# Optimization experiments

Hardware: AMD Instinct MI355X
Metric: run time of the kernel (lower is better)

The kernel has to match this reference:

```python
import jax, jax.numpy as jnp
import numpy as np

N_NODES = 100_000
N_EDGES = 800_000
D = 96
BN_EPS = 1e-5
LEAKY_SLOPE = 0.01


def setup_inputs() -> dict:
    key = jax.random.key(0)
    ks = jax.random.split(key, 9)
    x = jax.random.normal(ks[0], (N_NODES, D), dtype=jnp.float32)
    edge_index = jax.random.randint(ks[1], (2, N_EDGES), 0, N_NODES, dtype=jnp.int64)
    s = 0.05
    return {
        "x": x,
        "edge_index": edge_index,
        # SAGEConv #1 (mean aggregator, bias=False)
        "W_self1": jax.random.normal(ks[2], (D, D), dtype=jnp.float32) * s,
        "W_neigh1": jax.random.normal(ks[3], (D, D), dtype=jnp.float32) * s,
        # SAGEConv #2 (pool aggregator): fc_pool has bias, fc_self/fc_neigh bias=False
        "W_pool": jax.random.normal(ks[4], (D, D), dtype=jnp.float32) * s,
        "b_pool": jax.random.normal(ks[5], (D,), dtype=jnp.float32) * s,
        "W_self2": jax.random.normal(ks[6], (D, D), dtype=jnp.float32) * s,
        "W_neigh2": jax.random.normal(ks[7], (D, D), dtype=jnp.float32) * s,
        # BatchNorm affine params
        "g1": jnp.ones((D,), jnp.float32),
        "beta1": jnp.zeros((D,), jnp.float32),
        "g2": jnp.ones((D,), jnp.float32),
        "beta2": jnp.zeros((D,), jnp.float32),
    }


def _batch_norm(h, gamma, beta):
    # training-mode BatchNorm1d: biased batch stats over nodes
    mu = h.mean(axis=0)
    var = jnp.mean(jnp.square(h - mu), axis=0)
    return gamma * (h - mu) * jax.lax.rsqrt(var + BN_EPS) + beta


def _forward(x, edge_index, W_self1, W_neigh1, W_pool, b_pool, W_self2, W_neigh2,
             g1, beta1, g2, beta2):
    src, dst = edge_index[0], edge_index[1]
    n = x.shape[0]
    deg = jax.ops.segment_sum(jnp.ones((src.shape[0],), x.dtype), dst, num_segments=n)

    # ---- SAGEConv (mean): h_neigh = mean_{u in N(v)} x_u ; out = x W_self + h_neigh W_neigh
    agg_sum = jax.ops.segment_sum(x[src], dst, num_segments=n)          # [N, D]
    h_mean = agg_sum / jnp.maximum(deg, 1.0)[:, None]                   # 0 for isolated nodes
    out1 = x @ W_self1 + h_mean @ W_neigh1
    out1 = _batch_norm(out1, g1, beta1)

    # ---- SAGEConv (pool): h_neigh = max_{u in N(v)} relu(x_u W_pool + b_pool)
    hp = jax.nn.relu(x @ W_pool + b_pool)                               # [N, D]
    agg_max = jax.ops.segment_max(hp[src], dst, num_segments=n)        # -inf where empty
    h_max = jnp.where(deg[:, None] > 0, agg_max, 0.0)
    out2 = x @ W_self2 + h_max @ W_neigh2
    out2 = _batch_norm(out2, g2, beta2)

    return jax.nn.leaky_relu(out1 + out2, negative_slope=LEAKY_SLOPE)


def reference(x, edge_index, W_self1, W_neigh1, W_pool, b_pool, W_self2, W_neigh2,
              g1, beta1, g2, beta2):
    return _forward(x, edge_index, W_self1, W_neigh1, W_pool, b_pool,
                    W_self2, W_neigh2, g1, beta1, g2, beta2)
```

## Files before the change

kernel.cpp:

```cpp
#include <hip/hip_runtime.h>

#define NN 100000
#define NE 800000
#define DD 96
#define NROWPAD 100096
#define GBLK 782
#define SCAN_BLOCKS 100
#define SCAN_CHUNK 1000

typedef __attribute__((ext_vector_type(8))) short bf16x8;
typedef __attribute__((ext_vector_type(8))) unsigned short u16x8;
typedef __attribute__((ext_vector_type(4))) float f32x4;
typedef unsigned short u16;
typedef unsigned int u32;

#define MFMA16 __builtin_amdgcn_mfma_f32_16x16x32_bf16

#define OFF_DEG      0u
#define OFF_ROWSTART 100000u
#define OFF_CURSOR   200004u
#define OFF_BSUM     300004u
#define OFF_STATS    300132u
#define OFF_PARAMS   300516u
#define OFF_WT       300900u
#define OFF_CSR      323940u
#define OFF_XH       1123940u
#define OFF_HMBF     10733156u
#define OFF_HXBF     15537764u

__device__ __forceinline__ u16 f2b(float f) {
  u32 u = __float_as_uint(f);
  u += 0x7FFFu + ((u >> 16) & 1u);
  return (u16)(u >> 16);
}
__device__ __forceinline__ float b2f(short h) {
  return __uint_as_float(((u32)(u16)h) << 16);
}

__global__ void wprep_kernel(const float* __restrict__ Ws1, const float* __restrict__ Wn1,
                             const float* __restrict__ Ws2, const float* __restrict__ Wn2,
                             const float* __restrict__ Wp, u16* __restrict__ wt) {
  int idx = blockIdx.x * 256 + threadIdx.x;
  if (idx >= 5 * 9216) return;
  int m = idx / 9216, r = idx % 9216;
  int k = r / 96, c = r % 96;
  const float* W = (m == 0) ? Ws1 : (m == 1) ? Wn1 : (m == 2) ? Ws2 : (m == 3) ? Wn2 : Wp;
  wt[m * 9216 + c * 96 + k] = f2b(W[k * 96 + c]);
}

__global__ void deg_kernel(const int* __restrict__ dst, int* __restrict__ deg) {
  int e = blockIdx.x * blockDim.x + threadIdx.x;
  if (e >= NE) return;
  atomicAdd(&deg[dst[e]], 1);
}

__global__ void scan_sum_kernel(const int* __restrict__ deg, int* __restrict__ bsum) {
  __shared__ int red[256];
  int t = threadIdx.x;
  int base = blockIdx.x * SCAN_CHUNK;
  int s = 0;
  for (int i = t; i < SCAN_CHUNK; i += 256) s += deg[base + i];
  red[t] = s;
  __syncthreads();
  for (int off = 128; off > 0; off >>= 1) {
    if (t < off) red[t] += red[t + off];
    __syncthreads();
  }
  if (t == 0) bsum[blockIdx.x] = red[0];
}

__global__ void scan_bsum_kernel(int* __restrict__ bsum, int* __restrict__ row_start) {
  __shared__ int sm[128];
  int t = threadIdx.x;
  int v = (t < SCAN_BLOCKS) ? bsum[t] : 0;
  sm[t] = v;
  __syncthreads();
  for (int off = 1; off < 128; off <<= 1) {
    int u = 0;
    if (t >= off) u = sm[t - off];
    __syncthreads();
    if (t >= off) sm[t] += u;
    __syncthreads();
  }
  if (t < SCAN_BLOCKS) bsum[t] = sm[t] - v;
  if (t == SCAN_BLOCKS - 1) row_start[NN] = sm[t];
}

__global__ void scan_final_kernel(const int* __restrict__ deg,
                                  const int* __restrict__ bsum,
                                  int* __restrict__ row_start,
                                  int* __restrict__ cursor) {
  __shared__ int sm[256];
  int t = threadIdx.x;
  int base = blockIdx.x * SCAN_CHUNK + t * 4;
  int4 d = {0, 0, 0, 0};
  if (t < 250) d = *reinterpret_cast<const int4*>(deg + base);
  int tot = d.x + d.y + d.z + d.w;
  sm[t] = tot;
  __syncthreads();
  for (int off = 1; off < 256; off <<= 1) {
    int u = 0;
    if (t >= off) u = sm[t - off];
    __syncthreads();
    if (t >= off) sm[t] += u;
    __syncthreads();
  }
  if (t < 250) {
    int run = bsum[blockIdx.x] + sm[t] - tot;
    int4 rs;
    rs.x = run;
    rs.y = run + d.x;
    rs.z = run + d.x + d.y;
    rs.w = run + d.x + d.y + d.z;
    *reinterpret_cast<int4*>(row_start + base) = rs;
    *reinterpret_cast<int4*>(cursor + base) = rs;
  }
}

__global__ void fill_csr_kernel(const int* __restrict__ src,
                                const int* __restrict__ dst,
                                int* __restrict__ cursor,
                                int* __restrict__ csr) {
  int e = blockIdx.x * blockDim.x + threadIdx.x;
  if (e >= NE) return;
  int pos = atomicAdd(&cursor[dst[e]], 1);
  csr[pos] = src[e];
}

__global__ __launch_bounds__(512) void hp_gemm_kernel(const float* __restrict__ x,
                                                      const u16* __restrict__ wt,
                                                      const float* __restrict__ bp,
                                                      u16* __restrict__ xh) {
  __shared__ bf16x8 wl[1152];
  int t = threadIdx.x;
  const bf16x8* wg = reinterpret_cast<const bf16x8*>(wt + 4 * 9216);
  for (int j = t; j < 1152; j += 512) wl[j] = wg[j];
  __syncthreads();
  int w = t >> 6, lane = t & 63;
  int i = lane & 15, g = lane >> 4;
  int row_base = blockIdx.x * 128 + w * 16;
  int grow_a = row_base + i;
  int lrow = grow_a < NN ? grow_a : NN - 1;
  const float4* xr = reinterpret_cast<const float4*>(x + (size_t)lrow * 96);
  bf16x8* xhv = reinterpret_cast<bf16x8*>(xh);
  bf16x8 ax[3];
#pragma unroll
  for (int kb = 0; kb < 3; ++kb) {
    float4 p = xr[(kb * 4 + g) * 2];
    float4 q = xr[(kb * 4 + g) * 2 + 1];
    bf16x8 v;
    v[0] = (short)f2b(p.x); v[1] = (short)f2b(p.y); v[2] = (short)f2b(p.z); v[3] = (short)f2b(p.w);
    v[4] = (short)f2b(q.x); v[5] = (short)f2b(q.y); v[6] = (short)f2b(q.z); v[7] = (short)f2b(q.w);
    ax[kb] = v;
    xhv[(size_t)grow_a * 24 + kb * 4 + g] = v;
  }
  for (int nt = 0; nt < 6; ++nt) {
    f32x4 acc = {0.f, 0.f, 0.f, 0.f};
    int bch = (nt * 16 + i) * 12;
#pragma unroll
    for (int kb = 0; kb < 3; ++kb)
      acc = MFMA16(ax[kb], wl[bch + kb * 4 + g], acc, 0, 0, 0);
    int col = nt * 16 + i;
    float bias = bp[col];
#pragma unroll
    for (int r = 0; r < 4; ++r) {
      int grow = row_base + g * 4 + r;
      xh[(size_t)grow * 192 + 96 + col] = f2b(fmaxf(acc[r] + bias, 0.0f));
    }
  }
}

__global__ __launch_bounds__(256) void gather_kernel(const u16* __restrict__ xh,
                                                     const int* __restrict__ row_start,
                                                     const int* __restrict__ csr,
                                                     u16* __restrict__ hmbf,
                                                     u16* __restrict__ hxbf) {
  int t = threadIdx.x;
  int node = blockIdx.x * 32 + (t & 31);
  int slot = t >> 5;
  bool isMax = slot >= 4;
  if (node >= NN) return;
  int beg = row_start[node], end = row_start[node + 1];
  int cbase = slot * 3;
  const u16x8* XH = reinterpret_cast<const u16x8*>(xh);
  float s0[8], s1[8], s2[8];
  u16x8 m0, m1, m2;
#pragma unroll
  for (int j = 0; j < 8; ++j) {
    s0[j] = 0.f; s1[j] = 0.f; s2[j] = 0.f;
    m0[j] = 0; m1[j] = 0; m2[j] = 0;
  }
  int e = beg;
  int i0 = csr[(e < end) ? e : 0];
  int i1 = csr[(e + 1 < end) ? e + 1 : ((end > beg) ? end - 1 : 0)];
  for (; e + 2 <= end; e += 2) {
    int p2 = e + 2, p3 = e + 3;
    int n0 = csr[(p2 < end) ? p2 : end - 1];
    int n1 = csr[(p3 < end) ? p3 : end - 1];
    size_t b0 = (size_t)i0 * 24 + cbase;
    size_t b1 = (size_t)i1 * 24 + cbase;
    u16x8 u0 = XH[b0], u1 = XH[b0 + 1], u2 = XH[b0 + 2];
    u16x8 v0 = XH[b1], v1 = XH[b1 + 1], v2 = XH[b1 + 2];
    if (isMax) {
#pragma unroll
      for (int j = 0; j < 8; ++j) {
        u16 a = u0[j] > v0[j] ? u0[j] : v0[j]; m0[j] = m0[j] > a ? m0[j] : a;
        u16 b = u1[j] > v1[j] ? u1[j] : v1[j]; m1[j] = m1[j] > b ? m1[j] : b;
        u16 c = u2[j] > v2[j] ? u2[j] : v2[j]; m2[j] = m2[j] > c ? m2[j] : c;
      }
    } else {
#pragma unroll
      for (int j = 0; j < 8; ++j) {
        s0[j] += b2f((short)u0[j]) + b2f((short)v0[j]);
        s1[j] += b2f((short)u1[j]) + b2f((short)v1[j]);
        s2[j] += b2f((short)u2[j]) + b2f((short)v2[j]);
      }
    }
    i0 = n0; i1 = n1;
  }
  if (e < end) {
    size_t b0 = (size_t)i0 * 24 + cbase;
    u16x8 u0 = XH[b0], u1 = XH[b0 + 1], u2 = XH[b0 + 2];
    if (isMax) {
#pragma unroll
      for (int j = 0; j < 8; ++j) {
        m0[j] = m0[j] > u0[j] ? m0[j] : u0[j];
        m1[j] = m1[j] > u1[j] ? m1[j] : u1[j];
        m2[j] = m2[j] > u2[j] ? m2[j] : u2[j];
      }
    } else {
#pragma unroll
      for (int j = 0; j < 8; ++j) {
        s0[j] += b2f((short)u0[j]);
        s1[j] += b2f((short)u1[j]);
        s2[j] += b2f((short)u2[j]);
      }
    }
  }
  if (isMax) {
    u16x8* dv = reinterpret_cast<u16x8*>(hxbf);
    size_t ob = (size_t)node * 12 + (slot - 4) * 3;
    dv[ob] = m0; dv[ob + 1] = m1; dv[ob + 2] = m2;
  } else {
    float scl = (end > beg) ? 1.0f / (float)(end - beg) : 0.0f;
    u16x8 w0, w1, w2;
#pragma unroll
    for (int j = 0; j < 8; ++j) {
      w0[j] = f2b(s0[j] * scl);
      w1[j] = f2b(s1[j] * scl);
      w2[j] = f2b(s2[j] * scl);
    }
    u16x8* dv = reinterpret_cast<u16x8*>(hmbf);
    size_t ob = (size_t)node * 12 + slot * 3;
    dv[ob] = w0; dv[ob + 1] = w1; dv[ob + 2] = w2;
  }
}

__global__ __launch_bounds__(512, 4) void stats_gemm_kernel(const u16* __restrict__ xh,
                                                            const u16* __restrict__ hmbf,
                                                            const u16* __restrict__ hxbf,
                                                            const u16* __restrict__ wt,
                                                            float* __restrict__ stats) {
  __shared__ bf16x8 wl[4608];
  __shared__ float smst[384];
  int t = threadIdx.x;
  const bf16x8* wg = reinterpret_cast<const bf16x8*>(wt);
  for (int j = t; j < 4608; j += 512) wl[j] = wg[j];
  for (int j = t; j < 384; j += 512) smst[j] = 0.f;
  __syncthreads();
  int w = t >> 6, lane = t & 63;
  int i = lane & 15, g = lane >> 4;
  int row_base = blockIdx.x * 128 + w * 16;
  size_t arowx = (size_t)(row_base + i) * 24;
  size_t arowh = (size_t)(row_base + i) * 12;
  bf16x8 ax0, ax1, ax2, am0, am1, am2, ah0, ah1, ah2;
  {
    const bf16x8* X = reinterpret_cast<const bf16x8*>(xh);
    const bf16x8* M = reinterpret_cast<const bf16x8*>(hmbf);
    const bf16x8* H = reinterpret_cast<const bf16x8*>(hxbf);
    ax0 = X[arowx + g]; ax1 = X[arowx + 4 + g]; ax2 = X[arowx + 8 + g];
    am0 = M[arowh + g]; am1 = M[arowh + 4 + g]; am2 = M[arowh + 8 + g];
    ah0 = H[arowh + g]; ah1 = H[arowh + 4 + g]; ah2 = H[arowh + 8 + g];
  }
#pragma unroll
  for (int nt = 0; nt < 6; ++nt) {
    f32x4 a1 = {0.f, 0.f, 0.f, 0.f}, a2 = {0.f, 0.f, 0.f, 0.f};
    int bch = (nt * 16 + i) * 12 + g;
    a1 = MFMA16(ax0, wl[bch], a1, 0, 0, 0);
    a1 = MFMA16(ax1, wl[bch + 4], a1, 0, 0, 0);
    a1 = MFMA16(ax2, wl[bch + 8], a1, 0, 0, 0);
    a1 = MFMA16(am0, wl[1152 + bch], a1, 0, 0, 0);
    a1 = MFMA16(am1, wl[1152 + bch + 4], a1, 0, 0, 0);
    a1 = MFMA16(am2, wl[1152 + bch + 8], a1, 0, 0, 0);
    a2 = MFMA16(ax0, wl[2304 + bch], a2, 0, 0, 0);
    a2 = MFMA16(ax1, wl[2304 + bch + 4], a2, 0, 0, 0);
    a2 = MFMA16(ax2, wl[2304 + bch + 8], a2, 0, 0, 0);
    a2 = MFMA16(ah0, wl[3456 + bch], a2, 0, 0, 0);
    a2 = MFMA16(ah1, wl[3456 + bch + 4], a2, 0, 0, 0);
    a2 = MFMA16(ah2, wl[3456 + bch + 8], a2, 0, 0, 0);
    int col = nt * 16 + i;
    float s1 = 0, q1 = 0, s2 = 0, q2 = 0;
#pragma unroll
    for (int r = 0; r < 4; ++r) {
      int grow = row_base + g * 4 + r;
      if (grow < NN) {
        float v = a1[r], u = a2[r];
        s1 += v; q1 += v * v; s2 += u; q2 += u * u;
      }
    }
    s1 += __shfl_xor(s1, 16); q1 += __shfl_xor(q1, 16);
    s2 += __shfl_xor(s2, 16); q2 += __shfl_xor(q2, 16);
    s1 += __shfl_xor(s1, 32); q1 += __shfl_xor(q1, 32);
    s2 += __shfl_xor(s2, 32); q2 += __shfl_xor(q2, 32);
    if (g == 0) {
      atomicAdd(&smst[col], s1);
      atomicAdd(&smst[96 + col], q1);
      atomicAdd(&smst[192 + col], s2);
      atomicAdd(&smst[288 + col], q2);
    }
  }
  __syncthreads();
  for (int j = t; j < 384; j += 512) atomicAdd(&stats[j], smst[j]);
}

__global__ void finalize_kernel(const float* __restrict__ stats,
                                const float* __restrict__ g1, const float* __restrict__ beta1,
                                const float* __restrict__ g2, const float* __restrict__ beta2,
                                float* __restrict__ params) {
  int c = threadIdx.x;
  if (c >= 96) return;
  const float inv_n = 1.0f / NN;
  float mu1 = stats[c] * inv_n;
  float var1 = fmaxf(stats[96 + c] * inv_n - mu1 * mu1, 0.0f);
  float is1 = rsqrtf(var1 + 1e-5f);
  float a1 = g1[c] * is1;
  params[c] = a1;
  params[96 + c] = beta1[c] - a1 * mu1;
  float mu2 = stats[192 + c] * inv_n;
  float var2 = fmaxf(stats[288 + c] * inv_n - mu2 * mu2, 0.0f);
  float is2 = rsqrtf(var2 + 1e-5f);
  float a2 = g2[c] * is2;
  params[192 + c] = a2;
  params[288 + c] = beta2[c] - a2 * mu2;
}

__global__ __launch_bounds__(512, 4) void out_gemm_kernel(const u16* __restrict__ xh,
                                                          const u16* __restrict__ hmbf,
                                                          const u16* __restrict__ hxbf,
                                                          const u16* __restrict__ wt,
                                                          const float* __restrict__ params,
                                                          float* __restrict__ out) {
  __shared__ bf16x8 wl[4608];
  __shared__ float pl[384];
  int t = threadIdx.x;
  const bf16x8* wg = reinterpret_cast<const bf16x8*>(wt);
  for (int j = t; j < 4608; j += 512) wl[j] = wg[j];
  for (int j = t; j < 384; j += 512) pl[j] = params[j];
  __syncthreads();
  int w = t >> 6, lane = t & 63;
  int i = lane & 15, g = lane >> 4;
  int row_base = blockIdx.x * 128 + w * 16;
  size_t arowx = (size_t)(row_base + i) * 24;
  size_t arowh = (size_t)(row_base + i) * 12;
  bf16x8 ax0, ax1, ax2, am0, am1, am2, ah0, ah1, ah2;
  {
    const bf16x8* X = reinterpret_cast<const bf16x8*>(xh);
    const bf16x8* M = reinterpret_cast<const bf16x8*>(hmbf);
    const bf16x8* H = reinterpret_cast<const bf16x8*>(hxbf);
    ax0 = X[arowx + g]; ax1 = X[arowx + 4 + g]; ax2 = X[arowx + 8 + g];
    am0 = M[arowh + g]; am1 = M[arowh + 4 + g]; am2 = M[arowh + 8 + g];
    ah0 = H[arowh + g]; ah1 = H[arowh + 4 + g]; ah2 = H[arowh + 8 + g];
  }
#pragma unroll
  for (int nt = 0; nt < 6; ++nt) {
    f32x4 a1 = {0.f, 0.f, 0.f, 0.f}, a2 = {0.f, 0.f, 0.f, 0.f};
    int bch = (nt * 16 + i) * 12 + g;
    a1 = MFMA16(ax0, wl[bch], a1, 0, 0, 0);
    a1 = MFMA16(ax1, wl[bch + 4], a1, 0, 0, 0);
    a1 = MFMA16(ax2, wl[bch + 8], a1, 0, 0, 0);
    a1 = MFMA16(am0, wl[1152 + bch], a1, 0, 0, 0);
    a1 = MFMA16(am1, wl[1152 + bch + 4], a1, 0, 0, 0);
    a1 = MFMA16(am2, wl[1152 + bch + 8], a1, 0, 0, 0);
    a2 = MFMA16(ax0, wl[2304 + bch], a2, 0, 0, 0);
    a2 = MFMA16(ax1, wl[2304 + bch + 4], a2, 0, 0, 0);
    a2 = MFMA16(ax2, wl[2304 + bch + 8], a2, 0, 0, 0);
    a2 = MFMA16(ah0, wl[3456 + bch], a2, 0, 0, 0);
    a2 = MFMA16(ah1, wl[3456 + bch + 4], a2, 0, 0, 0);
    a2 = MFMA16(ah2, wl[3456 + bch + 8], a2, 0, 0, 0);
    int col = nt * 16 + i;
    float p1 = pl[col], c1 = pl[96 + col];
    float p2 = pl[192 + col], c2 = pl[288 + col];
#pragma unroll
    for (int r = 0; r < 4; ++r) {
      int grow = row_base + g * 4 + r;
      if (grow < NN) {
        float v = p1 * a1[r] + c1 + p2 * a2[r] + c2;
        v = v > 0.f ? v : 0.01f * v;
        out[(size_t)grow * 96 + col] = v;
      }
    }
  }
}

extern "C" void kernel_launch(void* const* d_in, const int* in_sizes, int n_in,
                              void* d_out, int out_size, void* d_ws, size_t ws_size,
                              hipStream_t stream) {
  const float* x       = (const float*)d_in[0];
  const int*   ei      = (const int*)d_in[1];
  const float* W_self1 = (const float*)d_in[2];
  const float* W_neigh1= (const float*)d_in[3];
  const float* W_pool  = (const float*)d_in[4];
  const float* b_pool  = (const float*)d_in[5];
  const float* W_self2 = (const float*)d_in[6];
  const float* W_neigh2= (const float*)d_in[7];
  const float* g1      = (const float*)d_in[8];
  const float* beta1   = (const float*)d_in[9];
  const float* g2      = (const float*)d_in[10];
  const float* beta2   = (const float*)d_in[11];
  float* out = (float*)d_out;

  float* ws = (float*)d_ws;
  int*   deg       = (int*)(ws + OFF_DEG);
  int*   row_start = (int*)(ws + OFF_ROWSTART);
  int*   cursor    = (int*)(ws + OFF_CURSOR);
  int*   bsum      = (int*)(ws + OFF_BSUM);
  float* stats     = ws + OFF_STATS;
  float* params    = ws + OFF_PARAMS;
  u16*   wt        = (u16*)(ws + OFF_WT);
  int*   csr       = (int*)(ws + OFF_CSR);
  u16*   xh        = (u16*)(ws + OFF_XH);
  u16*   hmbf      = (u16*)(ws + OFF_HMBF);
  u16*   hxbf      = (u16*)(ws + OFF_HXBF);

  const int* src = ei;
  const int* dst = ei + NE;

  hipMemsetAsync(deg, 0, NN * sizeof(int), stream);
  hipMemsetAsync(stats, 0, 384 * sizeof(float), stream);

  wprep_kernel<<<(5 * 9216 + 255) / 256, 256, 0, stream>>>(W_self1, W_neigh1, W_self2,
                                                           W_neigh2, W_pool, wt);

  deg_kernel<<<(NE + 255) / 256, 256, 0, stream>>>(dst, deg);
  scan_sum_kernel<<<SCAN_BLOCKS, 256, 0, stream>>>(deg, bsum);
  scan_bsum_kernel<<<1, 128, 0, stream>>>(bsum, row_start);
  scan_final_kernel<<<SCAN_BLOCKS, 256, 0, stream>>>(deg, bsum, row_start, cursor);
  fill_csr_kernel<<<(NE + 255) / 256, 256, 0, stream>>>(src, dst, cursor, csr);

  hp_gemm_kernel<<<GBLK, 512, 0, stream>>>(x, wt, b_pool, xh);

  gather_kernel<<<(NN + 31) / 32, 256, 0, stream>>>(xh, row_start, csr, hmbf, hxbf);

  stats_gemm_kernel<<<GBLK, 512, 0, stream>>>(xh, hmbf, hxbf, wt, stats);
  finalize_kernel<<<1, 128, 0, stream>>>(stats, g1, beta1, g2, beta2, params);
  out_gemm_kernel<<<GBLK, 512, 0, stream>>>(xh, hmbf, hxbf, wt, params, out);
}
```

Before: 268.9 us.

## Sort gather nodes by degree bucket to balance per-wavefront work

Adds a degree histogram, a 64-bin scan and a counting-sort pass that builds a node order grouped by in-degree, reusing the cursor slot after CSR fill. The gather kernel then processes nodes in that order, so the 32 nodes handled by a block have similar edge counts and lanes diverge less in the neighbor loop. It adds three small kernel launches, an extra indirection, and scattered output writes. Nodes within a degree bin land in atomic order, which can reduce locality of row_start and output accesses.

```diff
diff --git a/kernel.cpp b/kernel.cpp
--- a/kernel.cpp
+++ b/kernel.cpp
@@ -19,14 +19,16 @@
 #define OFF_DEG      0u
 #define OFF_ROWSTART 100000u
 #define OFF_CURSOR   200004u
+#define OFF_ORDER    200004u
 #define OFF_BSUM     300004u
-#define OFF_STATS    300132u
-#define OFF_PARAMS   300516u
-#define OFF_WT       300900u
-#define OFF_CSR      323940u
-#define OFF_XH       1123940u
-#define OFF_HMBF     10733156u
-#define OFF_HXBF     15537764u
+#define OFF_BINS     300132u
+#define OFF_STATS    300260u
+#define OFF_PARAMS   300644u
+#define OFF_WT       301028u
+#define OFF_CSR      324068u
+#define OFF_XH       1124068u
+#define OFF_HMBF     10733284u
+#define OFF_HXBF     15537892u
 
 __device__ __forceinline__ u16 f2b(float f) {
   u32 u = __float_as_uint(f);
@@ -127,6 +129,40 @@
   csr[pos] = src[e];
 }
 
+__global__ void dhist_kernel(const int* __restrict__ deg, int* __restrict__ bins) {
+  __shared__ int h[64];
+  int t = threadIdx.x;
+  if (t < 64) h[t] = 0;
+  __syncthreads();
+  int n = blockIdx.x * 256 + t;
+  if (n < NN) {
+    int d = deg[n]; if (d > 63) d = 63;
+    atomicAdd(&h[d], 1);
+  }
+  __syncthreads();
+  if (t < 64 && h[t]) atomicAdd(&bins[t], h[t]);
+}
+
+__global__ void bscan_kernel(const int* __restrict__ bins, int* __restrict__ bcur) {
+  int t = threadIdx.x;
+  int v = bins[t];
+  int s = v;
+  for (int off = 1; off < 64; off <<= 1) {
+    int u = __shfl_up(s, off);
+    if (t >= off) s += u;
+  }
+  bcur[t] = s - v;
+}
+
+__global__ void order_kernel(const int* __restrict__ deg, int* __restrict__ bcur,
+                             int* __restrict__ order) {
+  int n = blockIdx.x * 256 + threadIdx.x;
+  if (n >= NN) return;
+  int d = deg[n]; if (d > 63) d = 63;
+  int pos = atomicAdd(&bcur[d], 1);
+  order[pos] = n;
+}
+
 __global__ __launch_bounds__(512) void hp_gemm_kernel(const float* __restrict__ x,
                                                       const u16* __restrict__ wt,
                                                       const float* __restrict__ bp,
@@ -173,13 +209,14 @@
 __global__ __launch_bounds__(256) void gather_kernel(const u16* __restrict__ xh,
                                                      const int* __restrict__ row_start,
                                                      const int* __restrict__ csr,
+                                                     const int* __restrict__ order,
                                                      u16* __restrict__ hmbf,
                                                      u16* __restrict__ hxbf) {
   int t = threadIdx.x;
-  int node = blockIdx.x * 32 + (t & 31);
+  int idx = blockIdx.x * 32 + (t & 31);
+  int node = order[idx];
   int slot = t >> 5;
   bool isMax = slot >= 4;
-  if (node >= NN) return;
   int beg = row_start[node], end = row_start[node + 1];
   int cbase = slot * 3;
   const u16x8* XH = reinterpret_cast<const u16x8*>(xh);
@@ -423,7 +460,9 @@
   int*   deg       = (int*)(ws + OFF_DEG);
   int*   row_start = (int*)(ws + OFF_ROWSTART);
   int*   cursor    = (int*)(ws + OFF_CURSOR);
+  int*   order     = (int*)(ws + OFF_ORDER);
   int*   bsum      = (int*)(ws + OFF_BSUM);
+  int*   bins      = (int*)(ws + OFF_BINS);
   float* stats     = ws + OFF_STATS;
   float* params    = ws + OFF_PARAMS;
   u16*   wt        = (u16*)(ws + OFF_WT);
@@ -436,7 +475,7 @@
   const int* dst = ei + NE;
 
   hipMemsetAsync(deg, 0, NN * sizeof(int), stream);
-  hipMemsetAsync(stats, 0, 384 * sizeof(float), stream);
+  hipMemsetAsync(bins, 0, (128 + 384) * sizeof(float), stream);
 
   wprep_kernel<<<(5 * 9216 + 255) / 256, 256, 0, stream>>>(W_self1, W_neigh1, W_self2,
                                                            W_neigh2, W_pool, wt);
@@ -447,9 +486,13 @@
   scan_final_kernel<<<SCAN_BLOCKS, 256, 0, stream>>>(deg, bsum, row_start, cursor);
   fill_csr_kernel<<<(NE + 255) / 256, 256, 0, stream>>>(src, dst, cursor, csr);
 
+  dhist_kernel<<<(NN + 255) / 256, 256, 0, stream>>>(deg, bins);
+  bscan_kernel<<<1, 64, 0, stream>>>(bins, bins + 64);
+  order_kernel<<<(NN + 255) / 256, 256, 0, stream>>>(deg, bins + 64, order);
+
   hp_gemm_kernel<<<GBLK, 512, 0, stream>>>(x, wt, b_pool, xh);
 
-  gather_kernel<<<(NN + 31) / 32, 256, 0, stream>>>(xh, row_start, csr, hmbf, hxbf);
+  gather_kernel<<<(NN + 31) / 32, 256, 0, stream>>>(xh, row_start, csr, order, hmbf, hxbf);
 
   stats_gemm_kernel<<<GBLK, 512, 0, stream>>>(xh, hmbf, hxbf, wt, stats);
   finalize_kernel<<<1, 128, 0, stream>>>(stats, g1, beta1, g2, beta2, params);
```

Measured after the change: 633.4 us. +135.6%, slower.
